# Kernel optimization log

Measured on AMD Instinct MI355X. Metric: run time of the kernel, lower is better.

The kernel has to match this reference:

```python
import jax, jax.numpy as jnp
import numpy as np

SLOPE = 0.2
NEG = -9e15

def setup_inputs() -> dict:
    key = jax.random.key(0)
    k1, k2, k3, k4 = jax.random.split(key, 4)
    N, INP, OUT = 8192, 512, 128
    h = jax.random.normal(k1, (N, INP), dtype=jnp.float32)
    adj = jax.random.randint(k2, (N, N), 0, 2, dtype=jnp.int32)
    W = jax.random.normal(k3, (INP, OUT), dtype=jnp.float32) * (1.0 / np.sqrt(INP))
    a = jax.random.normal(k4, (2 * OUT,), dtype=jnp.float32) * (1.0 / np.sqrt(2 * OUT))
    return {"h": h, "adj": adj, "W": W, "a": a}

def reference(h, adj, W, a):
    OUT = W.shape[1]
    Wh = h @ W                               # [N, out]
    # a . [Wh_i, Wh_j] decomposes into two matvecs (same math as pairwise concat)
    f1 = Wh @ a[:OUT]                        # [N]
    f2 = Wh @ a[OUT:]                        # [N]
    e = jax.nn.leaky_relu(f1[:, None] + f2[None, :], negative_slope=SLOPE)  # [N, N]
    scores = jnp.where(adj > 0, e, NEG)
    attention = jax.nn.softmax(scores, axis=1)
    return attention @ Wh                    # [N, out]
```

## Files before the change

kernel.cpp:

```cpp
#include <hip/hip_runtime.h>

typedef unsigned short u16;
typedef unsigned int u32;
typedef __attribute__((ext_vector_type(8))) short short8v;
typedef __attribute__((ext_vector_type(4))) short short4v;
typedef __attribute__((ext_vector_type(4))) float float4v;
typedef __attribute__((ext_vector_type(4))) int   int4v;

#define N_NODES 8192
#define D_IN    512
#define D_OUT   128
#define SLOPEF  0.2f
#define LOG2E   1.4426950408889634f
#define NSEG    4
#define SEGCOLS 2048
#define NCHUNK  8

static __device__ __forceinline__ u16 f2bf(float f) {
    union { float f; unsigned int i; } v; v.f = f;
    unsigned int r = v.i + 0x7fff + ((v.i >> 16) & 1);
    return (u16)(r >> 16);
}
static __device__ __forceinline__ void lds_barrier() {
    asm volatile("s_waitcnt lgkmcnt(0)" ::: "memory");
    __builtin_amdgcn_s_barrier();
    asm volatile("" ::: "memory");
}

__global__ __launch_bounds__(256) void kc_convert(
        const float* __restrict__ h, const float* __restrict__ W,
        u16* __restrict__ hb, u16* __restrict__ WbT)
{
    if (blockIdx.x < 2048) {
        const size_t t = (size_t)blockIdx.x * 256 + threadIdx.x;
        const float4v* src = (const float4v*)h + t * 2;
        const float4v v0 = src[0], v1 = src[1];
        short8v o;
        o[0] = (short)f2bf(v0[0]); o[1] = (short)f2bf(v0[1]);
        o[2] = (short)f2bf(v0[2]); o[3] = (short)f2bf(v0[3]);
        o[4] = (short)f2bf(v1[0]); o[5] = (short)f2bf(v1[1]);
        o[6] = (short)f2bf(v1[2]); o[7] = (short)f2bf(v1[3]);
        *(short8v*)(hb + t * 8) = o;
    } else {
        const int t2 = (blockIdx.x - 2048) * 256 + threadIdx.x;
        const int k = t2 >> 4;
        const int n0 = (t2 & 15) * 8;
        const float4v* src = (const float4v*)(W + (size_t)k * D_OUT + n0);
        const float4v v0 = src[0], v1 = src[1];
        #pragma unroll
        for (int e = 0; e < 4; e++) WbT[(size_t)(n0 + e) * D_IN + k] = f2bf(v0[e]);
        #pragma unroll
        for (int e = 0; e < 4; e++) WbT[(size_t)(n0 + 4 + e) * D_IN + k] = f2bf(v1[e]);
    }
}

__global__ __launch_bounds__(256) void k1m_proj(
        const u16* __restrict__ hb, const u16* __restrict__ WbT,
        const float* __restrict__ a, u16* __restrict__ WhT,
        float* __restrict__ f1, float* __restrict__ f2)
{
    __shared__ short As[32 * 136];
    __shared__ short Ws[128 * 136];
    __shared__ float pf1[32][65];
    __shared__ float pf2[32][65];

    const int tid = threadIdx.x;
    const int rowbase = blockIdx.x * 32;
    const int lane = tid & 63, w = tid >> 6;
    const int quad = lane >> 4, m16 = lane & 15;

    float4v acc[2][2];
    #pragma unroll
    for (int mt = 0; mt < 2; mt++)
        #pragma unroll
        for (int nt = 0; nt < 2; nt++) {
            acc[mt][nt][0] = 0.f; acc[mt][nt][1] = 0.f;
            acc[mt][nt][2] = 0.f; acc[mt][nt][3] = 0.f;
        }

    for (int c = 0; c < 4; c++) {
        const int kc0 = c * 128;
        if (c) __syncthreads();
        {
            const int row = tid >> 3, koff = (tid & 7) * 16;
            const short8v* src = (const short8v*)(hb + (size_t)(rowbase + row) * D_IN + kc0 + koff);
            const short8v s0 = src[0], s1 = src[1];
            *(short8v*)&As[row * 136 + koff] = s0;
            *(short8v*)&As[row * 136 + koff + 8] = s1;
        }
        {
            const int n = tid & 127, h2 = tid >> 7;
            #pragma unroll
            for (int i = 0; i < 8; i++) {
                const int koff = h2 * 64 + i * 8;
                *(short8v*)&Ws[n * 136 + koff] =
                    *(const short8v*)(WbT + (size_t)n * D_IN + kc0 + koff);
            }
        }
        __syncthreads();
        #pragma unroll
        for (int ks = 0; ks < 4; ks++) {
            const int ko = ks * 32 + quad * 8;
            const short8v af0 = *(const short8v*)&As[m16 * 136 + ko];
            const short8v af1 = *(const short8v*)&As[(16 + m16) * 136 + ko];
            const short8v bf0 = *(const short8v*)&Ws[(w * 32 + m16) * 136 + ko];
            const short8v bf1 = *(const short8v*)&Ws[(w * 32 + 16 + m16) * 136 + ko];
            acc[0][0] = __builtin_amdgcn_mfma_f32_16x16x32_bf16(af0, bf0, acc[0][0], 0, 0, 0);
            acc[0][1] = __builtin_amdgcn_mfma_f32_16x16x32_bf16(af0, bf1, acc[0][1], 0, 0, 0);
            acc[1][0] = __builtin_amdgcn_mfma_f32_16x16x32_bf16(af1, bf0, acc[1][0], 0, 0, 0);
            acc[1][1] = __builtin_amdgcn_mfma_f32_16x16x32_bf16(af1, bf1, acc[1][1], 0, 0, 0);
        }
    }

    #pragma unroll
    for (int mt = 0; mt < 2; mt++) {
        #pragma unroll
        for (int nt = 0; nt < 2; nt++) {
            const int n = w * 32 + nt * 16 + m16;
            short4v p;
            #pragma unroll
            for (int reg = 0; reg < 4; reg++) p[reg] = (short)f2bf(acc[mt][nt][reg]);
            *(short4v*)(WhT + (size_t)n * N_NODES + rowbase + mt * 16 + quad * 4) = p;
        }
    }

    float a1v[2], a2v[2];
    #pragma unroll
    for (int nt = 0; nt < 2; nt++) {
        a1v[nt] = a[w * 32 + nt * 16 + m16];
        a2v[nt] = a[D_OUT + w * 32 + nt * 16 + m16];
    }
    #pragma unroll
    for (int mt = 0; mt < 2; mt++)
        #pragma unroll
        for (int reg = 0; reg < 4; reg++) {
            const int row = mt * 16 + quad * 4 + reg;
            pf1[row][w * 16 + m16] = acc[mt][0][reg] * a1v[0] + acc[mt][1][reg] * a1v[1];
            pf2[row][w * 16 + m16] = acc[mt][0][reg] * a2v[0] + acc[mt][1][reg] * a2v[1];
        }
    __syncthreads();
    if (tid < 32) {
        float s = 0.f;
        #pragma unroll
        for (int j = 0; j < 64; j++) s += pf1[tid][j];
        f1[rowbase + tid] = s * LOG2E;
    } else if (tid < 64) {
        float s = 0.f;
        #pragma unroll
        for (int j = 0; j < 64; j++) s += pf2[tid - 32][j];
        f2[rowbase + tid - 32] = s * LOG2E;
    }
}

__global__ __launch_bounds__(256, 3) void k2_attn(
        const int* __restrict__ adj, const u16* __restrict__ WhT,
        const float* __restrict__ f1g, const float* __restrict__ f2g,
        float* __restrict__ numw, float* __restrict__ denw)
{
    __shared__ short Pt[2][32 * 264];
    __shared__ float f2s[2304];
    __shared__ float f1s[32];
    __shared__ float rs[32][9];
    __shared__ float ssum[32];

    const int tid = threadIdx.x;
    const int rb  = blockIdx.x >> 2;
    const int seg = blockIdx.x & 3;
    const int rowbase = rb * 32;
    const int colbase = seg * SEGCOLS;
    const int r = tid >> 3, g = tid & 7;
    const int lane = tid & 63, w = tid >> 6;
    const int quad = lane >> 4, m16 = lane & 15;

    if (tid < 32) f1s[tid] = f1g[rowbase + tid];
    #pragma unroll
    for (int i = 0; i < 2; i++) {
        const int idx = (tid + 256 * i) * 4;
        *(float4v*)&f2s[idx + ((idx >> 5) << 2)] = *(const float4v*)&f2g[colbase + idx];
    }

    const int4v* arow = (const int4v*)(adj + (size_t)(rowbase + r) * N_NODES + colbase);
    int4v a4[8];
    #pragma unroll
    for (int i = 0; i < 8; i++) a4[i] = arow[g * 8 + i];

    float4v acc[2][2];
    #pragma unroll
    for (int mt = 0; mt < 2; mt++)
        #pragma unroll
        for (int nt = 0; nt < 2; nt++) {
            acc[mt][nt][0] = 0.f; acc[mt][nt][1] = 0.f;
            acc[mt][nt][2] = 0.f; acc[mt][nt][3] = 0.f;
        }
    float ls0 = 0.f, ls1 = 0.f, ls2 = 0.f, ls3 = 0.f;

    __syncthreads();

    const float f1v = f1s[r];

    auto weight_phase = [&](int jc, short* ptb) {
        const float* f2p = &f2s[jc * 288 + g * 36];
        u32 packed[16];
        #pragma unroll
        for (int i = 0; i < 8; i++) {
            const float4v fv = *(const float4v*)&f2p[i * 4];
            const int4v av = a4[i];
            u32 wb[4];
            #pragma unroll
            for (int e = 0; e < 4; e++) {
                const u32 msk = (av[e] > 0) ? 0xffff0000u : 0u;
                float x = f1v + fv[e];
                x = fmaxf(x, SLOPEF * x);
                const float ex = __builtin_amdgcn_exp2f(x);
                const u32 wt = __float_as_uint(ex) & msk;
                wb[e] = wt;
                if (e == 0) ls0 += __uint_as_float(wt);
                else if (e == 1) ls1 += __uint_as_float(wt);
                else if (e == 2) ls2 += __uint_as_float(wt);
                else ls3 += __uint_as_float(wt);
            }
            packed[i * 2]     = __builtin_amdgcn_perm(wb[1], wb[0], 0x07060302);
            packed[i * 2 + 1] = __builtin_amdgcn_perm(wb[3], wb[2], 0x07060302);
        }
        int* pdst = (int*)(ptb + r * 264 + g * 32);
        #pragma unroll
        for (int q = 0; q < 4; q++) {
            int4v st;
            st[0] = (int)packed[q * 4 + 0]; st[1] = (int)packed[q * 4 + 1];
            st[2] = (int)packed[q * 4 + 2]; st[3] = (int)packed[q * 4 + 3];
            *(int4v*)&pdst[q * 4] = st;
        }
    };

    weight_phase(0, Pt[0]);
    #pragma unroll
    for (int i = 0; i < 8; i++) a4[i] = arow[64 + g * 8 + i];

    #pragma unroll 2
    for (int jc = 0; jc < NCHUNK; jc++) {
        lds_barrier();

        {
            const u16* b0p = WhT + (size_t)(w * 32 + m16) * N_NODES + colbase + jc * 256 + quad * 8;
            const u16* b1p = b0p + 16 * N_NODES;
            const short* a0p = &Pt[jc & 1][m16 * 264 + quad * 8];
            const short* a1p = a0p + 16 * 264;
            #pragma unroll
            for (int ks = 0; ks < 8; ks++) {
                const int ko = ks * 32;
                const short8v af0 = *(const short8v*)(a0p + ko);
                const short8v af1 = *(const short8v*)(a1p + ko);
                const short8v bv0 = *(const short8v*)(b0p + ko);
                const short8v bv1 = *(const short8v*)(b1p + ko);
                acc[0][0] = __builtin_amdgcn_mfma_f32_16x16x32_bf16(af0, bv0, acc[0][0], 0, 0, 0);
                acc[0][1] = __builtin_amdgcn_mfma_f32_16x16x32_bf16(af0, bv1, acc[0][1], 0, 0, 0);
                acc[1][0] = __builtin_amdgcn_mfma_f32_16x16x32_bf16(af1, bv0, acc[1][0], 0, 0, 0);
                acc[1][1] = __builtin_amdgcn_mfma_f32_16x16x32_bf16(af1, bv1, acc[1][1], 0, 0, 0);
            }
        }
        if (jc + 1 < NCHUNK) {
            weight_phase(jc + 1, Pt[(jc + 1) & 1]);
            if (jc + 2 < NCHUNK) {
                #pragma unroll
                for (int i = 0; i < 8; i++) a4[i] = arow[(jc + 2) * 64 + g * 8 + i];
            }
        }
    }

    rs[r][g] = (ls0 + ls1) + (ls2 + ls3);
    __syncthreads();
    if (tid < 32) {
        float s = 0.f;
        #pragma unroll
        for (int j = 0; j < 8; j++) s += rs[tid][j];
        ssum[tid] = s;
        denw[(size_t)(rowbase + tid) * NSEG + seg] = s;
    }
    __syncthreads();

    #pragma unroll
    for (int mt = 0; mt < 2; mt++) {
        #pragma unroll
        for (int nt = 0; nt < 2; nt++) {
            const int cl = w * 32 + nt * 16 + m16;
            #pragma unroll
            for (int reg = 0; reg < 4; reg++) {
                const int rl = mt * 16 + quad * 4 + reg;
                numw[((size_t)(rowbase + rl) * NSEG + seg) * D_OUT + cl] = acc[mt][nt][reg];
            }
        }
    }
}

__global__ __launch_bounds__(256) void k3_reduce(
        const float* __restrict__ numw, const float* __restrict__ denw,
        float* __restrict__ out)
{
    const int tid = threadIdx.x;
    const int row = blockIdx.x * 2 + (tid >> 7);
    const int c   = tid & 127;
    float s = 0.f, d = 0.f;
    #pragma unroll
    for (int sg = 0; sg < NSEG; sg++) {
        s += numw[((size_t)row * NSEG + sg) * D_OUT + c];
        d += denw[(size_t)row * NSEG + sg];
    }
    out[(size_t)row * D_OUT + c] = s / d;
}

extern "C" void kernel_launch(void* const* d_in, const int* in_sizes, int n_in,
                              void* d_out, int out_size, void* d_ws, size_t ws_size,
                              hipStream_t stream) {
    const float* h   = (const float*)d_in[0];
    const int*   adj = (const int*)d_in[1];
    const float* W   = (const float*)d_in[2];
    const float* a   = (const float*)d_in[3];

    char* ws = (char*)d_ws;
    u16*   hb   = (u16*)ws;
    u16*   WbT  = (u16*)(ws + (size_t)8 * 1024 * 1024);
    u16*   WhT  = (u16*)(ws + (size_t)9 * 1024 * 1024);
    float* f1   = (float*)(ws + (size_t)11 * 1024 * 1024);
    float* f2   = f1 + N_NODES;
    float* numw = (float*)(ws + (size_t)12 * 1024 * 1024);
    float* denw = (float*)(ws + (size_t)28 * 1024 * 1024);

    kc_convert<<<2080, 256, 0, stream>>>(h, W, hb, WbT);
    k1m_proj<<<N_NODES / 32, 256, 0, stream>>>(hb, WbT, a, WhT, f1, f2);
    k2_attn<<<(N_NODES / 32) * NSEG, 256, 0, stream>>>(adj, WhT, f1, f2, numw, denw);
    k3_reduce<<<N_NODES / 2, 256, 0, stream>>>(numw, denw, (float*)d_out);
}
```

Before: 415.1 us.

## Double attention block rows to 64 to reuse WhT fragments across more tiles

The attention kernel now processes 64 rows per block with 128-column chunks instead of 32 rows with 256-column chunks. Each loaded WhT B-fragment feeds four MFMA row tiles rather than two, halving global/L2 traffic for WhT. The cost is doubled accumulator registers and a lower occupancy target (2 blocks per CU instead of 3), with half as many blocks in the grid.

```diff
diff --git a/kernel.cpp b/kernel.cpp
--- a/kernel.cpp
+++ b/kernel.cpp
@@ -14,7 +14,8 @@
 #define LOG2E   1.4426950408889634f
 #define NSEG    4
 #define SEGCOLS 2048
-#define NCHUNK  8
+#define NCHUNK  16
+#define ROWS    64
 
 static __device__ __forceinline__ u16 f2bf(float f) {
     union { float f; unsigned int i; } v; v.f = f;
@@ -152,27 +153,27 @@
     }
 }
 
-__global__ __launch_bounds__(256, 3) void k2_attn(
+__global__ __launch_bounds__(256, 2) void k2_attn(
         const int* __restrict__ adj, const u16* __restrict__ WhT,
         const float* __restrict__ f1g, const float* __restrict__ f2g,
         float* __restrict__ numw, float* __restrict__ denw)
 {
-    __shared__ short Pt[2][32 * 264];
+    __shared__ short Pt[2][ROWS * 136];
     __shared__ float f2s[2304];
-    __shared__ float f1s[32];
-    __shared__ float rs[32][9];
-    __shared__ float ssum[32];
+    __shared__ float f1s[ROWS];
+    __shared__ float rs[ROWS][5];
+    __shared__ float ssum[ROWS];
 
     const int tid = threadIdx.x;
     const int rb  = blockIdx.x >> 2;
     const int seg = blockIdx.x & 3;
-    const int rowbase = rb * 32;
+    const int rowbase = rb * ROWS;
     const int colbase = seg * SEGCOLS;
-    const int r = tid >> 3, g = tid & 7;
+    const int r = tid >> 2, g = tid & 3;
     const int lane = tid & 63, w = tid >> 6;
     const int quad = lane >> 4, m16 = lane & 15;
 
-    if (tid < 32) f1s[tid] = f1g[rowbase + tid];
+    if (tid < ROWS) f1s[tid] = f1g[rowbase + tid];
     #pragma unroll
     for (int i = 0; i < 2; i++) {
         const int idx = (tid + 256 * i) * 4;
@@ -184,9 +185,9 @@
     #pragma unroll
     for (int i = 0; i < 8; i++) a4[i] = arow[g * 8 + i];
 
-    float4v acc[2][2];
-    #pragma unroll
-    for (int mt = 0; mt < 2; mt++)
+    float4v acc[4][2];
+    #pragma unroll
+    for (int mt = 0; mt < 4; mt++)
         #pragma unroll
         for (int nt = 0; nt < 2; nt++) {
             acc[mt][nt][0] = 0.f; acc[mt][nt][1] = 0.f;
@@ -199,7 +200,7 @@
     const float f1v = f1s[r];
 
     auto weight_phase = [&](int jc, short* ptb) {
-        const float* f2p = &f2s[jc * 288 + g * 36];
+        const float* f2p = &f2s[jc * 144 + g * 36];
         u32 packed[16];
         #pragma unroll
         for (int i = 0; i < 8; i++) {
@@ -222,7 +223,7 @@
             packed[i * 2]     = __builtin_amdgcn_perm(wb[1], wb[0], 0x07060302);
             packed[i * 2 + 1] = __builtin_amdgcn_perm(wb[3], wb[2], 0x07060302);
         }
-        int* pdst = (int*)(ptb + r * 264 + g * 32);
+        int* pdst = (int*)(ptb + r * 136 + g * 32);
         #pragma unroll
         for (int q = 0; q < 4; q++) {
             int4v st;
@@ -234,52 +235,51 @@
 
     weight_phase(0, Pt[0]);
     #pragma unroll
-    for (int i = 0; i < 8; i++) a4[i] = arow[64 + g * 8 + i];
+    for (int i = 0; i < 8; i++) a4[i] = arow[32 + g * 8 + i];
 
     #pragma unroll 2
     for (int jc = 0; jc < NCHUNK; jc++) {
         lds_barrier();
 
         {
-            const u16* b0p = WhT + (size_t)(w * 32 + m16) * N_NODES + colbase + jc * 256 + quad * 8;
+            const u16* b0p = WhT + (size_t)(w * 32 + m16) * N_NODES + colbase + jc * 128 + quad * 8;
             const u16* b1p = b0p + 16 * N_NODES;
-            const short* a0p = &Pt[jc & 1][m16 * 264 + quad * 8];
-            const short* a1p = a0p + 16 * 264;
-            #pragma unroll
-            for (int ks = 0; ks < 8; ks++) {
+            const short* ap = &Pt[jc & 1][m16 * 136 + quad * 8];
+            #pragma unroll
+            for (int ks = 0; ks < 4; ks++) {
                 const int ko = ks * 32;
-                const short8v af0 = *(const short8v*)(a0p + ko);
-                const short8v af1 = *(const short8v*)(a1p + ko);
                 const short8v bv0 = *(const short8v*)(b0p + ko);
                 const short8v bv1 = *(const short8v*)(b1p + ko);
-                acc[0][0] = __builtin_amdgcn_mfma_f32_16x16x32_bf16(af0, bv0, acc[0][0], 0, 0, 0);
-                acc[0][1] = __builtin_amdgcn_mfma_f32_16x16x32_bf16(af0, bv1, acc[0][1], 0, 0, 0);
-                acc[1][0] = __builtin_amdgcn_mfma_f32_16x16x32_bf16(af1, bv0, acc[1][0], 0, 0, 0);
-                acc[1][1] = __builtin_amdgcn_mfma_f32_16x16x32_bf16(af1, bv1, acc[1][1], 0, 0, 0);
+                #pragma unroll
+                for (int mt = 0; mt < 4; mt++) {
+                    const short8v af = *(const short8v*)(ap + mt * 16 * 136 + ko);
+                    acc[mt][0] = __builtin_amdgcn_mfma_f32_16x16x32_bf16(af, bv0, acc[mt][0], 0, 0, 0);
+                    acc[mt][1] = __builtin_amdgcn_mfma_f32_16x16x32_bf16(af, bv1, acc[mt][1], 0, 0, 0);
+                }
             }
         }
         if (jc + 1 < NCHUNK) {
             weight_phase(jc + 1, Pt[(jc + 1) & 1]);
             if (jc + 2 < NCHUNK) {
                 #pragma unroll
-                for (int i = 0; i < 8; i++) a4[i] = arow[(jc + 2) * 64 + g * 8 + i];
+                for (int i = 0; i < 8; i++) a4[i] = arow[(jc + 2) * 32 + g * 8 + i];
             }
         }
     }
 
     rs[r][g] = (ls0 + ls1) + (ls2 + ls3);
     __syncthreads();
-    if (tid < 32) {
+    if (tid < ROWS) {
         float s = 0.f;
         #pragma unroll
-        for (int j = 0; j < 8; j++) s += rs[tid][j];
+        for (int j = 0; j < 4; j++) s += rs[tid][j];
         ssum[tid] = s;
         denw[(size_t)(rowbase + tid) * NSEG + seg] = s;
     }
     __syncthreads();
 
     #pragma unroll
-    for (int mt = 0; mt < 2; mt++) {
+    for (int mt = 0; mt < 4; mt++) {
         #pragma unroll
         for (int nt = 0; nt < 2; nt++) {
             const int cl = w * 32 + nt * 16 + m16;
@@ -327,6 +327,6 @@
 
     kc_convert<<<2080, 256, 0, stream>>>(h, W, hb, WbT);
     k1m_proj<<<N_NODES / 32, 256, 0, stream>>>(hb, WbT, a, WhT, f1, f2);
-    k2_attn<<<(N_NODES / 32) * NSEG, 256, 0, stream>>>(adj, WhT, f1, f2, numw, denw);
+    k2_attn<<<(N_NODES / ROWS) * NSEG, 256, 0, stream>>>(adj, WhT, f1, f2, numw, denw);
     k3_reduce<<<N_NODES / 2, 256, 0, stream>>>(numw, denw, (float*)d_out);
 }
```

Measured after the change: 397.7 us, median of 2. -4.2%, faster.
